# Kernel optimization log

Measured on AMD Instinct MI355X. Metric: run time of the kernel, lower is better.

The kernel has to match this reference:

```python
import jax, jax.numpy as jnp
import numpy as np

# Constants matching init_kwargs
PC_MIN_X, PC_MIN_Y = -70.4, -40.0
VX, VY = 0.1, 0.1
RADII = (0.4, 0.8)
NSAMPLE = 16
EPS = 1e-5

B, K, N = 2, 2048, 16384
C_BEV, H_BEV, W_BEV = 256, 100, 176


def setup_inputs() -> dict:
    key = jax.random.key(0)
    ks = jax.random.split(key, 16)
    u = lambda k, s: jax.random.uniform(k, s, jnp.float32)
    kp = jnp.stack([
        u(ks[0], (B, K)) * 136.0 - 68.0,
        u(ks[1], (B, K)) * 76.0 - 38.0,
        u(ks[2], (B, K)) * 2.5 - 2.0,   # z in (-2.0, 0.5) -> kpt_mask all True
    ], axis=-1)
    pts = jnp.stack([
        u(ks[3], (B, N)) * 140.0 - 70.0,
        u(ks[4], (B, N)) * 80.0 - 40.0,
        u(ks[5], (B, N)) * 4.0 - 3.0,
    ], axis=-1)
    r = lambda k, s: jax.random.normal(k, s, jnp.float32)
    s01 = lambda k, s: r(k, s) * 0.1
    return {
        "keypoints": kp,
        "points_xyz": pts,
        "points_feat": r(ks[6], (B, N, 1)),
        "spatial_features": r(ks[7], (B, C_BEV, H_BEV, W_BEV)),
        "bev_stride": 8,
        "W0_s0": s01(ks[8], (16, 4)), "g0_s0": jnp.ones(16), "b0_s0": jnp.zeros(16),
        "W1_s0": s01(ks[9], (16, 16)), "g1_s0": jnp.ones(16), "b1_s0": jnp.zeros(16),
        "W0_s1": s01(ks[10], (16, 4)), "g0_s1": jnp.ones(16), "b0_s1": jnp.zeros(16),
        "W1_s1": s01(ks[11], (32, 16)), "g1_s1": jnp.ones(32), "b1_s1": jnp.zeros(32),
        "Wf": s01(ks[12], (128, 304)), "gf": jnp.ones(128), "bf": jnp.zeros(128),
    }


def _batchnorm(x, g, b, axes):
    m = x.mean(axes, keepdims=True)
    v = x.var(axes, keepdims=True)
    return (x - m) * jax.lax.rsqrt(v + EPS) * g + b


def _ball_group(dist2, xyz_b, feat_b, kp_b, radius, ns):
    """pcdet ball_query: first ns in-radius neighbors (index order), pad by first idx."""
    Kq, Np = dist2.shape
    within = dist2 < radius * radius                      # (K, N)
    order = jnp.cumsum(within, axis=1) - 1                # slot for each point
    valid = within & (order < ns)
    pos = jnp.where(valid, order, ns)                     # invalid -> overflow slot
    idx = jnp.zeros((Kq, ns + 1), jnp.int32)
    idx = idx.at[jnp.arange(Kq)[:, None], pos].set(
        jnp.broadcast_to(jnp.arange(Np, dtype=jnp.int32)[None, :], (Kq, Np)))
    idx = idx[:, :ns]
    cnt = within.sum(axis=1)
    slot_ok = jnp.arange(ns)[None, :] < cnt[:, None]
    idx = jnp.where(slot_ok, idx, idx[:, :1])             # replicate first found idx
    empty = cnt == 0
    grouped_xyz = xyz_b[idx] - kp_b[:, None, :]           # (K, ns, 3)
    grouped = jnp.concatenate([grouped_xyz, feat_b[idx]], axis=-1)  # (K, ns, 3+C)
    grouped = jnp.where(empty[:, None, None], 0.0, grouped)
    return grouped, empty


def _group_both_scales(xyz_b, feat_b, kp_b):
    # pairwise dist computed ONCE, shared across both radii
    dist2 = jnp.sum((kp_b[:, None, :] - xyz_b[None, :, :]) ** 2, axis=-1)  # (K, N)
    g0, e0 = _ball_group(dist2, xyz_b, feat_b, kp_b, RADII[0], NSAMPLE)
    g1, e1 = _ball_group(dist2, xyz_b, feat_b, kp_b, RADII[1], NSAMPLE)
    return g0, e0, g1, e1


def _shared_mlp_pool(grouped, empty, layers):
    x = grouped                                            # (B, K, ns, Cin)
    for (W, g, b) in layers:
        x = jnp.einsum('bknc,oc->bkno', x, W)
        x = _batchnorm(x, g, b, axes=(0, 1, 2))            # BN2d over stacked M*ns
        x = jax.nn.relu(x)
    pooled = x.max(axis=2)                                 # max over ns -> (B, K, Cout)
    return jnp.where(empty[:, :, None], 0.0, pooled)


def _bev_interp(bev, kp, stride):
    # bev: (B, C, H, W); kp: (B, K, 3)
    im = jnp.transpose(bev, (0, 2, 3, 1))                  # (B, H, W, C)
    x = (kp[..., 0] - PC_MIN_X) / VX / stride
    y = (kp[..., 1] - PC_MIN_Y) / VY / stride
    Hh, Ww = im.shape[1], im.shape[2]
    x0 = jnp.clip(jnp.floor(x).astype(jnp.int32), 0, Ww - 1)
    x1 = jnp.clip(jnp.floor(x).astype(jnp.int32) + 1, 0, Ww - 1)
    y0 = jnp.clip(jnp.floor(y).astype(jnp.int32), 0, Hh - 1)
    y1 = jnp.clip(jnp.floor(y).astype(jnp.int32) + 1, 0, Hh - 1)
    bidx = jnp.arange(im.shape[0])[:, None]
    Ia, Ib = im[bidx, y0, x0], im[bidx, y1, x0]
    Ic, Id = im[bidx, y0, x1], im[bidx, y1, x1]
    x0f, x1f = x0.astype(x.dtype), x1.astype(x.dtype)
    y0f, y1f = y0.astype(y.dtype), y1.astype(y.dtype)
    wa = ((x1f - x) * (y1f - y))[..., None]
    wb = ((x1f - x) * (y - y0f))[..., None]
    wc = ((x - x0f) * (y1f - y))[..., None]
    wd = ((x - x0f) * (y - y0f))[..., None]
    return Ia * wa + Ib * wb + Ic * wc + Id * wd           # (B, K, C)


def reference(keypoints, points_xyz, points_feat, spatial_features, bev_stride,
              W0_s0, g0_s0, b0_s0, W1_s0, g1_s0, b1_s0,
              W0_s1, g0_s1, b0_s1, W1_s1, g1_s1, b1_s1,
              Wf, gf, bf):
    Bb, Kk, _ = keypoints.shape
    # BEV bilinear interpolation
    bev_feat = _bev_interp(spatial_features, keypoints, bev_stride)  # (B, K, C_bev)
    # per-batch ball-query grouping (vmapped over batch)
    g0, e0, g1, e1 = jax.vmap(_group_both_scales)(points_xyz, points_feat, keypoints)
    p0 = _shared_mlp_pool(g0, e0, [(W0_s0, g0_s0, b0_s0), (W1_s0, g1_s0, b1_s0)])
    p1 = _shared_mlp_pool(g1, e1, [(W0_s1, g0_s1, b0_s1), (W1_s1, g1_s1, b1_s1)])
    pooled = jnp.concatenate([p0, p1], axis=-1)            # (B, K, 48)
    feats = jnp.concatenate([bev_feat, pooled], axis=-1).reshape(Bb * Kk, -1)  # (M, 304)
    # vsa_point_feature_fusion: Linear(no bias) + BN1d(train) + ReLU
    fused = feats @ Wf.T
    fused = jax.nn.relu(_batchnorm(fused, gf, bf, axes=(0,)))
    return fused                                           # (B*K, 128)
```

## Files before the change

kernel.cpp:

```cpp
#include <hip/hip_runtime.h>
#include <hip/hip_bf16.h>

#define NB    2
#define NK    2048
#define NPTS  16384
#define NBK   4096
#define MSAMP 65536.0f
#define MROW  4096.0f

#define NCELLX 176
#define NCELLY 101
#define NCELLS 17776
#define CAP    24

#define NREP   16
#define NCTR   64

#define AL(p) __hip_atomic_load((p), __ATOMIC_RELAXED, __HIP_MEMORY_SCOPE_AGENT)

#define ATOMIC_ADD_ACK(p, v) do { \
  float _r = atomicAdd((p), (v)); \
  asm volatile("" :: "v"(_r)); } while (0)

#define ACC14(M, w, X, Y, Z, F) do { \
  M[0] += (w)*(X); M[1] += (w)*(Y); M[2] += (w)*(Z); M[3] += (w)*(F); \
  M[4] += (w)*(X)*(X); M[5] += (w)*(X)*(Y); M[6] += (w)*(X)*(Z); M[7] += (w)*(X)*(F); \
  M[8] += (w)*(Y)*(Y); M[9] += (w)*(Y)*(Z); M[10] += (w)*(Y)*(F); \
  M[11] += (w)*(Z)*(Z); M[12] += (w)*(Z)*(F); M[13] += (w)*(F)*(F); } while (0)

__device__ __forceinline__ int cell_of(float x, float y) {
  int cx = (int)floorf((x + 70.4f) * 1.25f);
  int cy = (int)floorf((y + 40.0f) * 1.25f);
  cx = min(max(cx, 0), NCELLX - 1);
  cy = min(max(cy, 0), NCELLY - 1);
  return cy * NCELLX + cx;
}

__device__ __forceinline__ void grid_barrier(int* ctrs, int per, int myc) {
  asm volatile("s_waitcnt vmcnt(0)" ::: "memory");
  __syncthreads();
  const int t = threadIdx.x;
  if (t == 0) {
    int old = __hip_atomic_fetch_add(&ctrs[myc], 1, __ATOMIC_RELAXED,
                                     __HIP_MEMORY_SCOPE_AGENT);
    asm volatile("" :: "v"(old));
  }
  if (t < NCTR) {
    while (__hip_atomic_load(&ctrs[t], __ATOMIC_RELAXED,
                             __HIP_MEMORY_SCOPE_AGENT) < per)
      __builtin_amdgcn_s_sleep(8);
  }
  __syncthreads();
}

__global__ __launch_bounds__(256) void bintrans_kernel(
    const float* __restrict__ pts, const float* __restrict__ pfeat,
    const float* __restrict__ bev,
    int* __restrict__ cellcnt, float4* __restrict__ bucketP,
    int* __restrict__ bucketI, float* __restrict__ bevT)
{
  __shared__ __align__(16) float ttile[64][65];
  const int t = threadIdx.x;
  const int wave = t >> 6;
  const int lane = t & 63;

  if (blockIdx.x < 128) {
    const int i  = blockIdx.x * 256 + t;
    const int b  = i >> 14;
    const int il = i & (NPTS - 1);
    const float* px = pts + (size_t)b * NPTS * 3;
    const float x = px[il*3+0], y = px[il*3+1], z = px[il*3+2];
    const float f = pfeat[(size_t)b * NPTS + il];
    const int c = b * NCELLS + cell_of(x, y);
    const int pos = atomicAdd(&cellcnt[c], 1);
    if (pos < CAP) {
      bucketP[(size_t)c * CAP + pos] = make_float4(x, y, z, f);
      bucketI[(size_t)c * CAP + pos] = il;
    }
    return;
  }

  const int tb  = blockIdx.x - 128;
  const int b   = tb / 1100;
  const int rem = tb % 1100;
  const int cg  = (rem / 275) * 64;
  const int sp0 = (rem % 275) * 64;
  #pragma unroll 4
  for (int i = 0; i < 16; i++) {
    const int c = cg + wave * 16 + i;
    ttile[wave * 16 + i][lane] = bev[((size_t)(b * 256 + c)) * 17600 + sp0 + lane];
  }
  __syncthreads();
  #pragma unroll 4
  for (int i = 0; i < 16; i++) {
    const int s = wave * 16 + i;
    bevT[((size_t)b * 17600 + sp0 + s) * 256 + cg + lane] = ttile[lane][s];
  }
}

__global__ __launch_bounds__(256, 2) void fused_kernel(
    const float* __restrict__ kp, const int* __restrict__ stridep,
    const float* __restrict__ bevT,
    const int* __restrict__ cellcnt, const float4* __restrict__ bucketP,
    const int* __restrict__ bucketI,
    const float* __restrict__ W0s0, const float* __restrict__ gm0s0, const float* __restrict__ bt0s0,
    const float* __restrict__ W0s1, const float* __restrict__ gm0s1, const float* __restrict__ bt0s1,
    const float* __restrict__ W1s0, const float* __restrict__ gm1s0, const float* __restrict__ bt1s0,
    const float* __restrict__ W1s1, const float* __restrict__ gm1s1, const float* __restrict__ bt1s1,
    const float* __restrict__ Wf, const float* __restrict__ gf, const float* __restrict__ bfp,
    float* __restrict__ S0r, float* __restrict__ S1r,
    float* __restrict__ S2sr, float* __restrict__ S2qr,
    int* __restrict__ ctrs, float* __restrict__ out)
{
  __shared__ float sW0a[64], sW0b[64], sW1a[256], sW1b[512], sP[160];
  __shared__ float skp[24];
  __shared__ float red[8][96];
  __shared__ float t2s[2][128], t2q[2][128];
  __shared__ float sA[128], sB[128];
  __shared__ __align__(16) float sF[8 * 304];
  __shared__ float4 sG0[8][16], sG1[8][16];
  __shared__ int scnt[2][8];
  const int t = threadIdx.x;
  const int bk0 = blockIdx.x * 8;
  const int rep = blockIdx.x & (NREP - 1);
  const int myc = blockIdx.x & (NCTR - 1);

  if (t < 24) skp[t] = kp[(size_t)bk0 * 3 + t];
  if (t < 64) { sW0a[t] = W0s0[t]; sW0b[t] = W0s1[t]; }
  sW1a[t]       = W1s0[t];
  sW1b[t]       = W1s1[t];
  sW1b[t + 256] = W1s1[t + 256];
  for (int i = t; i < 8 * 96; i += 256) ((float*)red)[i] = 0.f;
  __syncthreads();

  {
    const float st = (float)(*stridep);
    const int b = bk0 >> 11;
    const size_t pb = (size_t)b * 17600 * 256;
    #pragma unroll
    for (int r = 0; r < 8; r++) {
      const float x = (skp[r*3+0] - (-70.4f)) / 0.1f / st;
      const float y = (skp[r*3+1] - (-40.0f)) / 0.1f / st;
      const int xf = (int)floorf(x), yf = (int)floorf(y);
      const int x0 = min(max(xf, 0), 175), x1 = min(max(xf + 1, 0), 175);
      const int y0 = min(max(yf, 0), 99),  y1 = min(max(yf + 1, 0), 99);
      const float x0f = (float)x0, x1f = (float)x1, y0f = (float)y0, y1f = (float)y1;
      const float wa = (x1f - x) * (y1f - y);
      const float wb = (x1f - x) * (y - y0f);
      const float wc = (x - x0f) * (y1f - y);
      const float wd = (x - x0f) * (y - y0f);
      const float Ia = bevT[pb + (size_t)(y0 * 176 + x0) * 256 + t];
      const float Ib = bevT[pb + (size_t)(y1 * 176 + x0) * 256 + t];
      const float Ic = bevT[pb + (size_t)(y0 * 176 + x1) * 256 + t];
      const float Id = bevT[pb + (size_t)(y1 * 176 + x1) * 256 + t];
      sF[r * 304 + t] = Ia * wa + Ib * wb + Ic * wc + Id * wd;
    }
  }

  if (t < 8) {
    const int bk = bk0 + t;
    const int b  = bk >> 11;
    const float kx = skp[t*3+0], ky = skp[t*3+1], kz = skp[t*3+2];
    int cx = (int)floorf((kx + 70.4f) * 1.25f);
    int cy = (int)floorf((ky + 40.0f) * 1.25f);
    cx = min(max(cx, 1), NCELLX - 2);
    cy = min(max(cy, 1), NCELLY - 2);
    const int bcell = b * NCELLS;

    int c0 = 0, c1 = 0;
    int mi0 = 0x7fffffff, mi1 = 0x7fffffff;
    float p0x = 0.f, p0y = 0.f, p0z = 0.f, p0f = 0.f;
    float p1x = 0.f, p1y = 0.f, p1z = 0.f, p1f = 0.f;
    float M0[14], M1[14];
    #pragma unroll
    for (int i = 0; i < 14; i++) { M0[i] = 0.f; M1[i] = 0.f; }

    for (int dyc = -1; dyc <= 1; ++dyc) {
      const int rowbase = bcell + (cy + dyc) * NCELLX + cx - 1;
      for (int cc = 0; cc < 3; ++cc) {
        const int cell = rowbase + cc;
        const int n = min(cellcnt[cell], CAP);
        const float4* bp = bucketP + (size_t)cell * CAP;
        const int*    bi = bucketI + (size_t)cell * CAP;
        for (int j = 0; j < n; ++j) {
          const float4 p = bp[j];
          const float dx = p.x - kx, dy = p.y - ky, dz = p.z - kz;
          const float d2 = dx*dx + dy*dy + dz*dz;
          if (d2 < 0.64f) {
            const int pi = bi[j];
            if (c1 < 16) {
              sG1[t][c1] = make_float4(dx, dy, dz, p.w);
              ACC14(M1, 1.0f, dx, dy, dz, p.w);
            }
            if (pi < mi1) { mi1 = pi; p1x = dx; p1y = dy; p1z = dz; p1f = p.w; }
            c1++;
            if (d2 < 0.16f) {
              if (c0 < 16) {
                sG0[t][c0] = make_float4(dx, dy, dz, p.w);
                ACC14(M0, 1.0f, dx, dy, dz, p.w);
              }
              if (pi < mi0) { mi0 = pi; p0x = dx; p0y = dy; p0z = dz; p0f = p.w; }
              c0++;
            }
          }
        }
      }
    }

    {
      const float4 v0 = make_float4(p0x, p0y, p0z, p0f);
      for (int s2 = c0; s2 < 16; ++s2) sG0[t][s2] = v0;
      const float w0 = (float)(16 - min(c0, 16));
      ACC14(M0, w0, p0x, p0y, p0z, p0f);
    }
    {
      const float4 v1 = make_float4(p1x, p1y, p1z, p1f);
      for (int s2 = c1; s2 < 16; ++s2) sG1[t][s2] = v1;
      const float w1 = (float)(16 - min(c1, 16));
      ACC14(M1, w1, p1x, p1y, p1z, p1f);
    }
    scnt[0][t] = c0;
    scnt[1][t] = c1;

    #pragma unroll
    for (int d = 1; d < 8; d <<= 1) {
      #pragma unroll
      for (int i = 0; i < 14; i++) {
        M0[i] += __shfl_xor(M0[i], d);
        M1[i] += __shfl_xor(M1[i], d);
      }
    }
    if (t == 0) {
      float* S0my = S0r + rep * 32;
      #pragma unroll
      for (int i = 0; i < 14; i++) {
        ATOMIC_ADD_ACK(&S0my[i],      M0[i]);
        ATOMIC_ADD_ACK(&S0my[14 + i], M1[i]);
      }
    }
  }

  grid_barrier(ctrs, 512 / NCTR, myc);

  if (t < 32) {
    const int s = t >> 4, c = t & 15;
    const float* W  = s ? sW0b : sW0a;
    const float* G  = s ? gm0s1 : gm0s0;
    const float* Bt = s ? bt0s1 : bt0s0;
    const float w0 = W[c*4+0], w1 = W[c*4+1];
    const float w2 = W[c*4+2], w3 = W[c*4+3];
    const float inv = 1.0f / MSAMP;
    float Sv[14];
    #pragma unroll
    for (int i = 0; i < 14; i++) {
      float a = 0.f;
      #pragma unroll
      for (int r = 0; r < NREP; r++) a += AL(S0r + r * 32 + s * 14 + i);
      Sv[i] = a;
    }
    const float mean = (w0*Sv[0] + w1*Sv[1] + w2*Sv[2] + w3*Sv[3]) * inv;
    float e2 = w0*w0*Sv[4] + 2.f*w0*w1*Sv[5] + 2.f*w0*w2*Sv[6] + 2.f*w0*w3*Sv[7]
             + w1*w1*Sv[8] + 2.f*w1*w2*Sv[9] + 2.f*w1*w3*Sv[10]
             + w2*w2*Sv[11] + 2.f*w2*w3*Sv[12] + w3*w3*Sv[13];
    e2 *= inv;
    const float var = e2 - mean * mean;
    const float A = G[c] / sqrtf(var + 1e-5f);
    sP[s*32 + c]      = A;
    sP[s*32 + 16 + c] = Bt[c] - mean * A;
  }
  __syncthreads();

  if (t < 128) {
    const int lkp = t >> 4, sl = t & 15;
    const int grp = t >> 4;
    const bool leader = (t & 15) == 0;
    float a1[16];
    {
      const float4 x = sG0[lkp][sl];
      #pragma unroll
      for (int c = 0; c < 16; c++) {
        const float h = sW0a[c*4+0]*x.x + sW0a[c*4+1]*x.y + sW0a[c*4+2]*x.z + sW0a[c*4+3]*x.w;
        a1[c] = fmaxf(fmaf(sP[c], h, sP[16+c]), 0.f);
      }
      #pragma unroll
      for (int o = 0; o < 16; o++) {
        float h2 = 0.f;
        #pragma unroll
        for (int c = 0; c < 16; c++) h2 = fmaf(sW1a[o*16+c], a1[c], h2);
        float s = h2, q = h2 * h2;
        #pragma unroll
        for (int d = 1; d < 16; d <<= 1) { s += __shfl_xor(s, d); q += __shfl_xor(q, d); }
        if (leader) { red[grp][o] += s; red[grp][16+o] += q; }
      }
    }
    {
      const float4 x = sG1[lkp][sl];
      #pragma unroll
      for (int c = 0; c < 16; c++) {
        const float h = sW0b[c*4+0]*x.x + sW0b[c*4+1]*x.y + sW0b[c*4+2]*x.z + sW0b[c*4+3]*x.w;
        a1[c] = fmaxf(fmaf(sP[32+c], h, sP[48+c]), 0.f);
      }
      #pragma unroll
      for (int o = 0; o < 32; o++) {
        float h2 = 0.f;
        #pragma unroll
        for (int c = 0; c < 16; c++) h2 = fmaf(sW1b[o*16+c], a1[c], h2);
        float s = h2, q = h2 * h2;
        #pragma unroll
        for (int d = 1; d < 16; d <<= 1) { s += __shfl_xor(s, d); q += __shfl_xor(q, d); }
        if (leader) { red[grp][32+o] += s; red[grp][64+o] += q; }
      }
    }
  }
  __syncthreads();
  if (t < 96) {
    float s = 0.f;
    #pragma unroll
    for (int g = 0; g < 8; g++) s += red[g][t];
    ATOMIC_ADD_ACK(&S1r[rep * 96 + t], s);
  }

  grid_barrier(ctrs + NCTR, 512 / NCTR, myc);

  if (t < 48) {
    float sum = 0.f, sq = 0.f, G, Bv; int oA, oB, os, oq;
    if (t < 16) { os = t; oq = 16 + t; G = gm1s0[t]; Bv = bt1s0[t]; oA = 64+t;  oB = 80+t; }
    else { const int c = t - 16; os = 32 + c; oq = 64 + c; G = gm1s1[c]; Bv = bt1s1[c]; oA = 96+c; oB = 128+c; }
    #pragma unroll
    for (int r = 0; r < NREP; r++) {
      sum += AL(S1r + r * 96 + os);
      sq  += AL(S1r + r * 96 + oq);
    }
    const float mean = sum / MSAMP;
    const float var  = sq / MSAMP - mean * mean;
    const float A = G / sqrtf(var + 1e-5f);
    sP[oA] = A;
    sP[oB] = Bv - mean * A;
  }
  __syncthreads();

  if (t < 128) {
    const int lkp = t >> 4, slot = t & 15;
    float a1[16], a2s0[16], a2s1[32];
    {
      const float4 x = sG0[lkp][slot];
      #pragma unroll
      for (int c = 0; c < 16; c++) {
        const float h = sW0a[c*4+0]*x.x + sW0a[c*4+1]*x.y + sW0a[c*4+2]*x.z + sW0a[c*4+3]*x.w;
        a1[c] = fmaxf(fmaf(sP[c], h, sP[16+c]), 0.f);
      }
      #pragma unroll
      for (int o = 0; o < 16; o++) {
        float h2 = 0.f;
        #pragma unroll
        for (int c = 0; c < 16; c++) h2 = fmaf(sW1a[o*16+c], a1[c], h2);
        a2s0[o] = fmaxf(fmaf(sP[64+o], h2, sP[80+o]), 0.f);
      }
    }
    {
      const float4 x = sG1[lkp][slot];
      #pragma unroll
      for (int c = 0; c < 16; c++) {
        const float h = sW0b[c*4+0]*x.x + sW0b[c*4+1]*x.y + sW0b[c*4+2]*x.z + sW0b[c*4+3]*x.w;
        a1[c] = fmaxf(fmaf(sP[32+c], h, sP[48+c]), 0.f);
      }
      #pragma unroll
      for (int o = 0; o < 32; o++) {
        float h2 = 0.f;
        #pragma unroll
        for (int c = 0; c < 16; c++) h2 = fmaf(sW1b[o*16+c], a1[c], h2);
        a2s1[o] = fmaxf(fmaf(sP[96+o], h2, sP[128+o]), 0.f);
      }
    }
    #pragma unroll
    for (int d = 1; d < 16; d <<= 1) {
      #pragma unroll
      for (int o = 0; o < 16; o++) a2s0[o] = fmaxf(a2s0[o], __shfl_xor(a2s0[o], d));
      #pragma unroll
      for (int o = 0; o < 32; o++) a2s1[o] = fmaxf(a2s1[o], __shfl_xor(a2s1[o], d));
    }
    if (slot == 0) {
      const int c0 = scnt[0][lkp], c1 = scnt[1][lkp];
      float* outp = sF + lkp * 304 + 256;
      #pragma unroll
      for (int o = 0; o < 16; o++) outp[o] = c0 ? a2s0[o] : 0.f;
      #pragma unroll
      for (int o = 0; o < 32; o++) outp[16 + o] = c1 ? a2s1[o] : 0.f;
    }
  }
  __syncthreads();

  const int c = t & 127;
  const int half = t >> 7;
  const int rbase = half * 4;
  float acc[4];
  {
    #pragma unroll
    for (int r = 0; r < 4; r++) acc[r] = 0.f;
    const float* wrow = Wf + (size_t)c * 304;
    for (int j4 = 0; j4 < 76; j4++) {
      const float4 w = *(const float4*)(wrow + j4 * 4);
      #pragma unroll
      for (int r = 0; r < 4; r++) {
        const float4 f = *(const float4*)(sF + (rbase + r) * 304 + j4 * 4);
        acc[r] = fmaf(w.x, f.x, acc[r]);
        acc[r] = fmaf(w.y, f.y, acc[r]);
        acc[r] = fmaf(w.z, f.z, acc[r]);
        acc[r] = fmaf(w.w, f.w, acc[r]);
      }
    }
    float s = 0.f, q = 0.f;
    #pragma unroll
    for (int r = 0; r < 4; r++) {
      s += acc[r];
      q = fmaf(acc[r], acc[r], q);
    }
    t2s[half][c] = s;
    t2q[half][c] = q;
  }
  __syncthreads();
  if (t < 128) {
    ATOMIC_ADD_ACK(&S2sr[rep * 128 + t], t2s[0][t] + t2s[1][t]);
    ATOMIC_ADD_ACK(&S2qr[rep * 128 + t], t2q[0][t] + t2q[1][t]);
  }

  grid_barrier(ctrs + 2 * NCTR, 512 / NCTR, myc);

  if (t < 128) {
    float s = 0.f, q = 0.f;
    #pragma unroll
    for (int r = 0; r < NREP; r++) {
      s += AL(S2sr + r * 128 + t);
      q += AL(S2qr + r * 128 + t);
    }
    const float mean = s / MROW;
    const float var  = q / MROW - mean * mean;
    const float A = gf[t] / sqrtf(var + 1e-5f);
    sA[t] = A;
    sB[t] = bfp[t] - mean * A;
  }
  __syncthreads();
  {
    const float A = sA[c], B = sB[c];
    #pragma unroll
    for (int r = 0; r < 4; r++) {
      out[(size_t)(bk0 + rbase + r) * 128 + c] = fmaxf(fmaf(acc[r], A, B), 0.f);
    }
  }
}

extern "C" void kernel_launch(void* const* d_in, const int* in_sizes, int n_in,
                              void* d_out, int out_size, void* d_ws, size_t ws_size,
                              hipStream_t stream)
{
  const float* kp    = (const float*)d_in[0];
  const float* pts   = (const float*)d_in[1];
  const float* pfeat = (const float*)d_in[2];
  const float* bev   = (const float*)d_in[3];
  const int*   strd  = (const int*)d_in[4];
  const float* W0s0  = (const float*)d_in[5];
  const float* g0s0  = (const float*)d_in[6];
  const float* b0s0  = (const float*)d_in[7];
  const float* W1s0  = (const float*)d_in[8];
  const float* g1s0  = (const float*)d_in[9];
  const float* b1s0  = (const float*)d_in[10];
  const float* W0s1  = (const float*)d_in[11];
  const float* g0s1  = (const float*)d_in[12];
  const float* b0s1  = (const float*)d_in[13];
  const float* W1s1  = (const float*)d_in[14];
  const float* g1s1  = (const float*)d_in[15];
  const float* b1s1  = (const float*)d_in[16];
  const float* Wf    = (const float*)d_in[17];
  const float* gf    = (const float*)d_in[18];
  const float* bfv   = (const float*)d_in[19];

  float* w = (float*)d_ws;
  int*   cellcnt = (int*)(w + 1048576);
  int*   ctrs    = cellcnt + 2 * NCELLS;
  float* S0r     = (float*)(ctrs + 3 * NCTR);
  float* S1r     = S0r + NREP * 32;
  float* S2sr    = S1r + NREP * 96;
  float* S2qr    = S2sr + NREP * 128;
  const size_t zero_elems = 2 * NCELLS + 3 * NCTR + NREP * (32 + 96 + 128 + 128);

  float*  bevT    = w + 1245184;
  float4* bucketP = (float4*)(w + 10256384);
  int*    bucketI = (int*)(w + 10256384 + (size_t)2 * NCELLS * CAP * 4);

  hipMemsetAsync(cellcnt, 0, zero_elems * sizeof(int), stream);
  hipLaunchKernelGGL(bintrans_kernel, dim3(2328), dim3(256), 0, stream,
                     pts, pfeat, bev, cellcnt, bucketP, bucketI, bevT);
  hipLaunchKernelGGL(fused_kernel, dim3(512), dim3(256), 0, stream,
                     kp, strd, bevT, cellcnt, bucketP, bucketI,
                     W0s0, g0s0, b0s0, W0s1, g0s1, b0s1,
                     W1s0, g1s0, b1s0, W1s1, g1s1, b1s1,
                     Wf, gf, bfv, S0r, S1r, S2sr, S2qr, ctrs, (float*)d_out);
}
```

Before: 217.0 us.

## Use master-block release grid barrier, double reduction replicas, prefetch cell counts

```diff
diff --git a/kernel.cpp b/kernel.cpp
--- a/kernel.cpp
+++ b/kernel.cpp
@@ -13,7 +13,7 @@
 #define NCELLS 17776
 #define CAP    24
 
-#define NREP   16
+#define NREP   32
 #define NCTR   64
 
 #define AL(p) __hip_atomic_load((p), __ATOMIC_RELAXED, __HIP_MEMORY_SCOPE_AGENT)
@@ -36,19 +36,29 @@
   return cy * NCELLX + cx;
 }
 
-__device__ __forceinline__ void grid_barrier(int* ctrs, int per, int myc) {
+__device__ __forceinline__ void grid_barrier(int* base, int per, int myc) {
   asm volatile("s_waitcnt vmcnt(0)" ::: "memory");
   __syncthreads();
   const int t = threadIdx.x;
+  int* ctr = base;
+  int* rel = base + NCTR;
   if (t == 0) {
-    int old = __hip_atomic_fetch_add(&ctrs[myc], 1, __ATOMIC_RELAXED,
+    int old = __hip_atomic_fetch_add(&ctr[myc], 1, __ATOMIC_RELAXED,
                                      __HIP_MEMORY_SCOPE_AGENT);
     asm volatile("" :: "v"(old));
   }
-  if (t < NCTR) {
-    while (__hip_atomic_load(&ctrs[t], __ATOMIC_RELAXED,
-                             __HIP_MEMORY_SCOPE_AGENT) < per)
-      __builtin_amdgcn_s_sleep(8);
+  if (blockIdx.x == 0) {
+    if (t < NCTR) {
+      while (AL(&ctr[t]) < per) __builtin_amdgcn_s_sleep(8);
+    }
+    __syncthreads();
+    if (t < NCTR)
+      __hip_atomic_store(&rel[t], 1, __ATOMIC_RELAXED,
+                         __HIP_MEMORY_SCOPE_AGENT);
+  } else {
+    if (t == 0) {
+      while (AL(&rel[myc]) == 0) __builtin_amdgcn_s_sleep(8);
+    }
   }
   __syncthreads();
 }
@@ -166,6 +176,14 @@
     cx = min(max(cx, 1), NCELLX - 2);
     cy = min(max(cy, 1), NCELLY - 2);
     const int bcell = b * NCELLS;
+    const int cb0 = bcell + (cy - 1) * NCELLX + cx - 1;
+
+    int ncnt[9];
+    #pragma unroll
+    for (int r = 0; r < 3; r++)
+      #pragma unroll
+      for (int cc = 0; cc < 3; cc++)
+        ncnt[r*3+cc] = min(cellcnt[cb0 + r * NCELLX + cc], CAP);
 
     int c0 = 0, c1 = 0;
     int mi0 = 0x7fffffff, mi1 = 0x7fffffff;
@@ -175,11 +193,12 @@
     #pragma unroll
     for (int i = 0; i < 14; i++) { M0[i] = 0.f; M1[i] = 0.f; }
 
-    for (int dyc = -1; dyc <= 1; ++dyc) {
-      const int rowbase = bcell + (cy + dyc) * NCELLX + cx - 1;
-      for (int cc = 0; cc < 3; ++cc) {
-        const int cell = rowbase + cc;
-        const int n = min(cellcnt[cell], CAP);
+    #pragma unroll
+    for (int r = 0; r < 3; r++) {
+      #pragma unroll
+      for (int cc = 0; cc < 3; cc++) {
+        const int cell = cb0 + r * NCELLX + cc;
+        const int n = ncnt[r*3+cc];
         const float4* bp = bucketP + (size_t)cell * CAP;
         const int*    bi = bucketI + (size_t)cell * CAP;
         for (int j = 0; j < n; ++j) {
@@ -320,7 +339,7 @@
     ATOMIC_ADD_ACK(&S1r[rep * 96 + t], s);
   }
 
-  grid_barrier(ctrs + NCTR, 512 / NCTR, myc);
+  grid_barrier(ctrs + 2 * NCTR, 512 / NCTR, myc);
 
   if (t < 48) {
     float sum = 0.f, sq = 0.f, G, Bv; int oA, oB, os, oq;
@@ -424,7 +443,7 @@
     ATOMIC_ADD_ACK(&S2qr[rep * 128 + t], t2q[0][t] + t2q[1][t]);
   }
 
-  grid_barrier(ctrs + 2 * NCTR, 512 / NCTR, myc);
+  grid_barrier(ctrs + 4 * NCTR, 512 / NCTR, myc);
 
   if (t < 128) {
     float s = 0.f, q = 0.f;
@@ -477,11 +496,12 @@
   float* w = (float*)d_ws;
   int*   cellcnt = (int*)(w + 1048576);
   int*   ctrs    = cellcnt + 2 * NCELLS;
-  float* S0r     = (float*)(ctrs + 3 * NCTR);
+  float* S0r     = (float*)(ctrs + 6 * NCTR);
   float* S1r     = S0r + NREP * 32;
   float* S2sr    = S1r + NREP * 96;
   float* S2qr    = S2sr + NREP * 128;
-  const size_t zero_elems = 2 * NCELLS + 3 * NCTR + NREP * (32 + 96 + 128 + 128);
+  const size_t zero_elems = 2 * NCELLS + 6 * NCTR
+                          + NREP * (32 + 96 + 128 + 128);
 
   float*  bevT    = w + 1245184;
   float4* bucketP = (float4*)(w + 10256384);
```

Measured after the change: 191.1 us. -11.9%, faster.
